# Optimization experiments

Measured on AMD Instinct MI355X. Metric: run time of the kernel, lower is better.

Reference implementation:

```python
import jax, jax.numpy as jnp
import numpy as np
import math

B, S, H = 2, 2048, 2048
NH, LD = 16, 512
HD = H // NH


def setup_inputs() -> dict:
    key = jax.random.key(0)
    ks = jax.random.split(key, 9)
    sc = 0.02
    return {
        "x": jax.random.normal(ks[0], (B, S, H), dtype=jnp.float32),
        "wq": jax.random.normal(ks[1], (H, H), dtype=jnp.float32) * sc,
        "bq": jnp.zeros((H,), dtype=jnp.float32),
        "wk_lat": jax.random.normal(ks[2], (H, LD), dtype=jnp.float32) * sc,
        "wv_lat": jax.random.normal(ks[3], (H, LD), dtype=jnp.float32) * sc,
        "wk": jax.random.normal(ks[4], (LD, H), dtype=jnp.float32) * sc,
        "wv": jax.random.normal(ks[5], (LD, H), dtype=jnp.float32) * sc,
        "wo": jax.random.normal(ks[6], (H, H), dtype=jnp.float32) * sc,
        "bo": jnp.zeros((H,), dtype=jnp.float32),
    }


def reference(x, wq, bq, wk_lat, wv_lat, wk, wv, wo, bo):
    b, s, _ = x.shape
    # projections
    q = (x @ wq + bq).reshape(b, s, NH, HD).transpose(0, 2, 1, 3)  # [B,NH,S,HD]
    k_lat = x @ wk_lat  # [B,S,LD]
    v_lat = x @ wv_lat
    k = (k_lat @ wk).reshape(b, s, NH, HD).transpose(0, 2, 1, 3)
    v = (v_lat @ wv).reshape(b, s, NH, HD).transpose(0, 2, 1, 3)
    # causal attention
    scores = jnp.einsum('bhqd,bhkd->bhqk', q, k) / math.sqrt(HD)
    mask = jnp.tril(jnp.ones((s, s), dtype=bool))  # True = keep
    scores = jnp.where(mask, scores, -jnp.inf)
    weights = jax.nn.softmax(scores, axis=-1)
    out = jnp.einsum('bhqk,bhkd->bhqd', weights, v)
    out = out.transpose(0, 2, 1, 3).reshape(b, s, H)
    return out @ wo + bo
```

## Files before the change

### kernel.cpp

```cpp
#include <hip/hip_runtime.h>
#include <hip/hip_bf16.h>

#define PB   2
#define PS   2048
#define PH   2048
#define PNH  16
#define PLD  512
#define PHD  128
#define PM   (PB * PS)
#define PNCAT 3072
#define ATT_SCALE 0.08838834764831845f
#define ATT_MOFF 4.0f

typedef __attribute__((ext_vector_type(8))) short bf16x8;
typedef __attribute__((ext_vector_type(4))) float f32x4;

__device__ __forceinline__ unsigned short f2bf(float f) {
    unsigned int u = __float_as_uint(f);
    u += 0x7FFFu + ((u >> 16) & 1u);
    return (unsigned short)(u >> 16);
}

__device__ __forceinline__ void gl_lds16(const unsigned short* g, unsigned short* l) {
    __builtin_amdgcn_global_load_lds(
        (const __attribute__((address_space(1))) unsigned int*)g,
        (__attribute__((address_space(3))) unsigned int*)l, 16, 0, 0);
}

#define VMCNT(n)     asm volatile("s_waitcnt vmcnt(" #n ")" ::: "memory")

__global__ __launch_bounds__(256) void cast_f32_bf16_kernel(
    const float* __restrict__ in, unsigned short* __restrict__ out, int n)
{
    int i = (blockIdx.x * 256 + threadIdx.x) * 4;
    if (i >= n) return;
    float4 f = *(const float4*)(in + i);
    unsigned int a = (unsigned int)f2bf(f.x) | ((unsigned int)f2bf(f.y) << 16);
    unsigned int b = (unsigned int)f2bf(f.z) | ((unsigned int)f2bf(f.w) << 16);
    *(uint2*)(out + i) = make_uint2(a, b);
}

__global__ __launch_bounds__(256) void transpose_cast_kernel(
    const float* __restrict__ in, unsigned short* __restrict__ out, int R, int C)
{
    __shared__ float tile[32][33];
    int tx = threadIdx.x, ty = threadIdx.y;
    int r0 = blockIdx.y * 32, c0 = blockIdx.x * 32;
#pragma unroll
    for (int i = 0; i < 32; i += 8)
        tile[ty + i][tx] = in[(size_t)(r0 + ty + i) * C + (c0 + tx)];
    __syncthreads();
#pragma unroll
    for (int i = 0; i < 32; i += 8)
        out[(size_t)(c0 + ty + i) * R + (r0 + tx)] = f2bf(tile[tx][ty + i]);
}

template<int EPI, bool HAS_BIAS>
__global__ __launch_bounds__(256, 3) void gemm97_kernel(
    const unsigned short* __restrict__ A, int lda,
    const unsigned short* __restrict__ BT,
    const float* __restrict__ bias, int nbias,
    void* __restrict__ Cout, int ldc, int K)
{
    __shared__ __align__(16) unsigned short As[128 * 64];
    __shared__ __align__(16) unsigned short Bs[128 * 64];

    const int tid  = threadIdx.x;
    const int wave = tid >> 6, lane = tid & 63;
    const int wm = wave >> 1, wn = wave & 1;
    const int quad = lane >> 4, l15 = lane & 15;
    const int sw = l15 & 7;

    const int gx  = gridDim.x;
    const int nwg = gx * gridDim.y;
    int wg = blockIdx.y * gx + blockIdx.x;
    if (!(nwg & 7)) wg = (wg & 7) * (nwg >> 3) + (wg >> 3);
    const int bm = (wg / gx) * 128, bn = (wg % gx) * 128;

    const int nt = K >> 6;

    const int srow = tid >> 3;
    const int scol = ((tid & 7) ^ (srow & 7)) << 3;
    const unsigned short* Ag = A  + (size_t)(bm + srow) * lda + scol;
    const unsigned short* Bg = BT + (size_t)(bn + srow) * K   + scol;
    unsigned short* const ldsA = &As[wave * 512];
    unsigned short* const ldsB = &Bs[wave * 512];

    auto ldA = [&](int m, int ks) -> bf16x8 {
        int ra = wm * 64 + m * 16 + l15;
        return *(const bf16x8*)&As[ra * 64 + (((ks * 4 + quad) ^ sw) << 3)];
    };
    auto ldB = [&](int j, int ks) -> bf16x8 {
        int rb = wn * 64 + j * 16 + l15;
        return *(const bf16x8*)&Bs[rb * 64 + (((ks * 4 + quad) ^ sw) << 3)];
    };

    f32x4 acc[4][4] = {};

    for (int kt = 0; kt < nt; ++kt) {
        const int k0 = kt * 64;
#pragma unroll
        for (int s = 0; s < 4; ++s) {
            gl_lds16(Ag + (size_t)(s * 32) * lda + k0, ldsA + s * 2048);
            gl_lds16(Bg + (size_t)(s * 32) * K   + k0, ldsB + s * 2048);
        }
        VMCNT(0);
        __syncthreads();

        bf16x8 bfr[4][2];
#pragma unroll
        for (int j = 0; j < 4; ++j)
#pragma unroll
            for (int ks = 0; ks < 2; ++ks) bfr[j][ks] = ldB(j, ks);
#pragma unroll
        for (int m = 0; m < 4; ++m) {
            bf16x8 a0 = ldA(m, 0), a1 = ldA(m, 1);
#pragma unroll
            for (int j = 0; j < 4; ++j) {
                acc[m][j] = __builtin_amdgcn_mfma_f32_16x16x32_bf16(a0, bfr[j][0], acc[m][j], 0, 0, 0);
                acc[m][j] = __builtin_amdgcn_mfma_f32_16x16x32_bf16(a1, bfr[j][1], acc[m][j], 0, 0, 0);
            }
        }
        __syncthreads();
    }

#pragma unroll
    for (int m = 0; m < 4; ++m)
#pragma unroll
        for (int j = 0; j < 4; ++j)
#pragma unroll
            for (int r = 0; r < 4; ++r) {
                int row = bm + wm * 64 + m * 16 + quad * 4 + r;
                int col = bn + wn * 64 + j * 16 + l15;
                float val = acc[m][j][r];
                if (HAS_BIAS && col < nbias) val += bias[col];
                if (EPI == 2) {
                    int bb = row >> 11, s = row & 2047, hh = col >> 7, d = col & 127;
                    size_t idx = ((size_t)((bb << 4) + hh) << 18) + ((size_t)(s >> 6) << 13)
                               + ((d >> 3) << 9) + ((s & 63) << 3) + (d & 7);
                    ((unsigned short*)Cout)[idx] = f2bf(val);
                } else if (EPI == 3) {
                    int bb = row >> 11, s = row & 2047, hh = col >> 7, d = col & 127;
                    size_t idx = ((size_t)((bb << 4) + hh) << 18) + ((size_t)(s >> 6) << 13)
                               + (((s >> 3) & 7) << 10) + (d << 3) + (s & 7);
                    ((unsigned short*)Cout)[idx] = f2bf(val);
                } else if (EPI == 1) {
                    ((float*)Cout)[(size_t)row * ldc + col] = val;
                } else {
                    ((unsigned short*)Cout)[(size_t)row * ldc + col] = f2bf(val);
                }
            }
}

__global__ __launch_bounds__(256) void flash_attn_mfma_kernel(
    const unsigned short* __restrict__ q,
    const unsigned short* __restrict__ kswz,
    const unsigned short* __restrict__ vswz,
    unsigned short* __restrict__ o)
{
    __shared__ __align__(16) unsigned short Kl[2][8192];
    __shared__ __align__(16) unsigned short Vl[8192];
    __shared__ __align__(16) unsigned short Ps[4][16][72];

    const int tid  = threadIdx.x;
    const int wave = tid >> 6;
    const int lane = tid & 63;
    const int quad = lane >> 4, l15 = lane & 15;

    const int bid = blockIdx.x;
    const int qt = 31 - (bid >> 5);
    const int bh = bid & 31;
    const int b  = bh >> 4, h = bh & 15;
    const int q0 = qt * 64;

    const unsigned short* qbase = q + (size_t)(b * PS + q0) * PNCAT + h * PHD;
    const unsigned short* kbase = kswz + ((size_t)bh << 18);
    const unsigned short* vbase = vswz + ((size_t)bh << 18);

    auto stageK = [&](int it, int buf) {
        const unsigned short* kt = kbase + ((size_t)it << 13);
#pragma unroll
        for (int j = 0; j < 4; ++j)
            gl_lds16(kt + (wave * 4 + j) * 512 + lane * 8, &Kl[buf][(wave * 4 + j) * 512]);
    };
    auto stageV = [&](int it) {
        const unsigned short* vt = vbase + ((size_t)it << 13);
#pragma unroll
        for (int j = 0; j < 4; ++j)
            gl_lds16(vt + (wave * 4 + j) * 512 + lane * 8, &Vl[(wave * 4 + j) * 512]);
    };

    bf16x8 aq[4];
#pragma unroll
    for (int kk = 0; kk < 4; ++kk)
        aq[kk] = *(const bf16x8*)(qbase + (size_t)(wave * 16 + l15) * PNCAT + kk * 32 + quad * 8);

    bf16x8 vones;
#pragma unroll
    for (int j = 0; j < 8; ++j) vones[j] = (short)0x3F80;

    f32x4 oacc[8] = {};
    f32x4 lacc = {};

    stageK(0, 0);

    for (int it = 0; it <= qt; ++it) {
        const int cur = it & 1;
        __syncthreads();
        stageV(it);
        if (it < qt) stageK(it + 1, cur ^ 1);

        f32x4 sacc[4] = {};
#pragma unroll
        for (int kk = 0; kk < 4; ++kk)
#pragma unroll
            for (int n = 0; n < 4; ++n) {
                bf16x8 bk = *(const bf16x8*)&Kl[cur][((kk * 4 + quad) * 64 + n * 16 + l15) * 8];
                sacc[n] = __builtin_amdgcn_mfma_f32_16x16x32_bf16(aq[kk], bk, sacc[n], 0, 0, 0);
            }

        const bool diag = (it == qt);
#pragma unroll
        for (int n = 0; n < 4; ++n)
#pragma unroll
            for (int r = 0; r < 4; ++r) {
                float p = __expf(fmaf(sacc[n][r], ATT_SCALE, -ATT_MOFF));
                if (diag && (n * 16 + l15 > wave * 16 + quad * 4 + r)) p = 0.0f;
                Ps[wave][quad * 4 + r][n * 16 + l15] = f2bf(p);
            }

        __syncthreads();

#pragma unroll
        for (int kk = 0; kk < 2; ++kk) {
            bf16x8 ap = *(const bf16x8*)&Ps[wave][l15][kk * 32 + quad * 8];
            lacc = __builtin_amdgcn_mfma_f32_16x16x32_bf16(ap, vones, lacc, 0, 0, 0);
#pragma unroll
            for (int n = 0; n < 8; ++n) {
                bf16x8 bv = *(const bf16x8*)&Vl[((kk * 4 + quad) * 128 + n * 16 + l15) * 8];
                oacc[n] = __builtin_amdgcn_mfma_f32_16x16x32_bf16(ap, bv, oacc[n], 0, 0, 0);
            }
        }
    }

    float inv[4];
#pragma unroll
    for (int r = 0; r < 4; ++r) inv[r] = 1.0f / lacc[r];
#pragma unroll
    for (int n = 0; n < 8; ++n)
#pragma unroll
        for (int r = 0; r < 4; ++r) {
            int row = q0 + wave * 16 + quad * 4 + r;
            int col = h * PHD + n * 16 + l15;
            o[(size_t)(b * PS + row) * PH + col] = f2bf(oacc[n][r] * inv[r]);
        }
}

extern "C" void kernel_launch(void* const* d_in, const int* in_sizes, int n_in,
                              void* d_out, int out_size, void* d_ws, size_t ws_size,
                              hipStream_t stream)
{
    const float* x      = (const float*)d_in[0];
    const float* wq     = (const float*)d_in[1];
    const float* bq     = (const float*)d_in[2];
    const float* wk_lat = (const float*)d_in[3];
    const float* wv_lat = (const float*)d_in[4];
    const float* wk     = (const float*)d_in[5];
    const float* wv     = (const float*)d_in[6];
    const float* wo     = (const float*)d_in[7];
    const float* bo     = (const float*)d_in[8];
    float* out = (float*)d_out;

    char* ws = (char*)d_ws;
    size_t off = 0;
    auto alloc = [&](size_t bytes) -> void* {
        void* p = ws + off;
        off += (bytes + 255) & ~(size_t)255;
        return p;
    };
    unsigned short* xb    = (unsigned short*)alloc((size_t)PM * PH * 2);
    unsigned short* wcatT = (unsigned short*)alloc((size_t)PNCAT * PH * 2);
    unsigned short* wkT   = (unsigned short*)alloc((size_t)PH * PLD * 2);
    unsigned short* wvT   = (unsigned short*)alloc((size_t)PH * PLD * 2);
    unsigned short* woT   = (unsigned short*)alloc((size_t)PH * PH * 2);
    unsigned short* cat   = (unsigned short*)alloc((size_t)PM * PNCAT * 2);
    unsigned short* kswz  = (unsigned short*)alloc((size_t)PM * PH * 2);
    unsigned short* attn  = (unsigned short*)alloc((size_t)PM * PH * 2);
    unsigned short* vswz  = xb;

    unsigned short* wqT    = wcatT;
    unsigned short* wkLatT = wcatT + (size_t)PH * PH;
    unsigned short* wvLatT = wcatT + (size_t)(PH + PLD) * PH;

    dim3 tb(32, 8);

    cast_f32_bf16_kernel<<<(PM * PH) / 4 / 256, 256, 0, stream>>>(x, xb, PM * PH);
    transpose_cast_kernel<<<dim3(PH / 32,  PH / 32),  tb, 0, stream>>>(wq,     wqT,    PH,  PH);
    transpose_cast_kernel<<<dim3(PLD / 32, PH / 32),  tb, 0, stream>>>(wk_lat, wkLatT, PH,  PLD);
    transpose_cast_kernel<<<dim3(PLD / 32, PH / 32),  tb, 0, stream>>>(wv_lat, wvLatT, PH,  PLD);
    transpose_cast_kernel<<<dim3(PH / 32,  PLD / 32), tb, 0, stream>>>(wk,     wkT,    PLD, PH);
    transpose_cast_kernel<<<dim3(PH / 32,  PLD / 32), tb, 0, stream>>>(wv,     wvT,    PLD, PH);
    transpose_cast_kernel<<<dim3(PH / 32,  PH / 32),  tb, 0, stream>>>(wo,     woT,    PH,  PH);

    gemm97_kernel<0, true><<<dim3(PNCAT / 128, PM / 128), 256, 0, stream>>>(
        xb, PH, wcatT, bq, PH, cat, PNCAT, PH);

    gemm97_kernel<2, false><<<dim3(PH / 128, PM / 128), 256, 0, stream>>>(
        cat + PH, PNCAT, wkT, nullptr, 0, kswz, 0, PLD);
    gemm97_kernel<3, false><<<dim3(PH / 128, PM / 128), 256, 0, stream>>>(
        cat + PH + PLD, PNCAT, wvT, nullptr, 0, vswz, 0, PLD);

    flash_attn_mfma_kernel<<<PB * PNH * (PS / 64), 256, 0, stream>>>(cat, kswz, vswz, attn);

    gemm97_kernel<1, true><<<dim3(PH / 128, PM / 128), 256, 0, stream>>>(
        attn, PH, woT, bo, PH, out, PH, PH);
}
```

Baseline: 343.5 us.

## Single-buffer K in attention for occupancy, use exp2, batch weight transposes into one launch

The attention kernel drops double-buffered K staging and loads K and V together at the start of each tile. This shrinks LDS so three blocks can fit per CU, as the new launch bounds request, but it gives up the K prefetch overlap. The exponent now uses exp2f with pre-scaled constants, and the Ps row padding goes from 72 to 76. The six weight transpose-cast launches are merged into one 3D-grid kernel that reads its parameters from a struct, cutting launch overhead at the cost of early-exiting blocks for the smaller matrices.

```diff
diff --git a/kernel.cpp b/kernel.cpp
--- a/kernel.cpp
+++ b/kernel.cpp
@@ -11,6 +11,8 @@
 #define PNCAT 3072
 #define ATT_SCALE 0.08838834764831845f
 #define ATT_MOFF 4.0f
+#define ATT_SC2  0.12751744f
+#define ATT_MO2  5.77078016f
 
 typedef __attribute__((ext_vector_type(8))) short bf16x8;
 typedef __attribute__((ext_vector_type(4))) float f32x4;
@@ -28,6 +30,7 @@
 }
 
 #define VMCNT(n)     asm volatile("s_waitcnt vmcnt(" #n ")" ::: "memory")
+#define MEMFENCE()   asm volatile("" ::: "memory")
 
 __global__ __launch_bounds__(256) void cast_f32_bf16_kernel(
     const float* __restrict__ in, unsigned short* __restrict__ out, int n)
@@ -40,12 +43,23 @@
     *(uint2*)(out + i) = make_uint2(a, b);
 }
 
-__global__ __launch_bounds__(256) void transpose_cast_kernel(
-    const float* __restrict__ in, unsigned short* __restrict__ out, int R, int C)
+struct TC6 {
+    const float* src[6];
+    unsigned short* dst[6];
+    int R[6];
+    int C[6];
+};
+
+__global__ __launch_bounds__(256) void transpose_cast6_kernel(TC6 p)
 {
     __shared__ float tile[32][33];
+    const int z = blockIdx.z;
+    const int r0 = blockIdx.y * 32, c0 = blockIdx.x * 32;
+    const int R = p.R[z], C = p.C[z];
+    if (r0 >= R || c0 >= C) return;
+    const float* in = p.src[z];
+    unsigned short* out = p.dst[z];
     int tx = threadIdx.x, ty = threadIdx.y;
-    int r0 = blockIdx.y * 32, c0 = blockIdx.x * 32;
 #pragma unroll
     for (int i = 0; i < 32; i += 8)
         tile[ty + i][tx] = in[(size_t)(r0 + ty + i) * C + (c0 + tx)];
@@ -152,15 +166,15 @@
             }
 }
 
-__global__ __launch_bounds__(256) void flash_attn_mfma_kernel(
+__global__ __launch_bounds__(256, 3) void flash_attn_mfma_kernel(
     const unsigned short* __restrict__ q,
     const unsigned short* __restrict__ kswz,
     const unsigned short* __restrict__ vswz,
     unsigned short* __restrict__ o)
 {
-    __shared__ __align__(16) unsigned short Kl[2][8192];
+    __shared__ __align__(16) unsigned short Kl[8192];
     __shared__ __align__(16) unsigned short Vl[8192];
-    __shared__ __align__(16) unsigned short Ps[4][16][72];
+    __shared__ __align__(16) unsigned short Ps[4][16][76];
 
     const int tid  = threadIdx.x;
     const int wave = tid >> 6;
@@ -177,11 +191,11 @@
     const unsigned short* kbase = kswz + ((size_t)bh << 18);
     const unsigned short* vbase = vswz + ((size_t)bh << 18);
 
-    auto stageK = [&](int it, int buf) {
+    auto stageK = [&](int it) {
         const unsigned short* kt = kbase + ((size_t)it << 13);
 #pragma unroll
         for (int j = 0; j < 4; ++j)
-            gl_lds16(kt + (wave * 4 + j) * 512 + lane * 8, &Kl[buf][(wave * 4 + j) * 512]);
+            gl_lds16(kt + (wave * 4 + j) * 512 + lane * 8, &Kl[(wave * 4 + j) * 512]);
     };
     auto stageV = [&](int it) {
         const unsigned short* vt = vbase + ((size_t)it << 13);
@@ -202,20 +216,20 @@
     f32x4 oacc[8] = {};
     f32x4 lacc = {};
 
-    stageK(0, 0);
-
     for (int it = 0; it <= qt; ++it) {
-        const int cur = it & 1;
         __syncthreads();
+        stageK(it);
         stageV(it);
-        if (it < qt) stageK(it + 1, cur ^ 1);
+        VMCNT(4);
+        __builtin_amdgcn_s_barrier();
+        MEMFENCE();
 
         f32x4 sacc[4] = {};
 #pragma unroll
         for (int kk = 0; kk < 4; ++kk)
 #pragma unroll
             for (int n = 0; n < 4; ++n) {
-                bf16x8 bk = *(const bf16x8*)&Kl[cur][((kk * 4 + quad) * 64 + n * 16 + l15) * 8];
+                bf16x8 bk = *(const bf16x8*)&Kl[((kk * 4 + quad) * 64 + n * 16 + l15) * 8];
                 sacc[n] = __builtin_amdgcn_mfma_f32_16x16x32_bf16(aq[kk], bk, sacc[n], 0, 0, 0);
             }
 
@@ -224,7 +238,7 @@
         for (int n = 0; n < 4; ++n)
 #pragma unroll
             for (int r = 0; r < 4; ++r) {
-                float p = __expf(fmaf(sacc[n][r], ATT_SCALE, -ATT_MOFF));
+                float p = exp2f(fmaf(sacc[n][r], ATT_SC2, -ATT_MO2));
                 if (diag && (n * 16 + l15 > wave * 16 + quad * 4 + r)) p = 0.0f;
                 Ps[wave][quad * 4 + r][n * 16 + l15] = f2bf(p);
             }
@@ -292,15 +306,16 @@
     unsigned short* wkLatT = wcatT + (size_t)PH * PH;
     unsigned short* wvLatT = wcatT + (size_t)(PH + PLD) * PH;
 
-    dim3 tb(32, 8);
-
     cast_f32_bf16_kernel<<<(PM * PH) / 4 / 256, 256, 0, stream>>>(x, xb, PM * PH);
-    transpose_cast_kernel<<<dim3(PH / 32,  PH / 32),  tb, 0, stream>>>(wq,     wqT,    PH,  PH);
-    transpose_cast_kernel<<<dim3(PLD / 32, PH / 32),  tb, 0, stream>>>(wk_lat, wkLatT, PH,  PLD);
-    transpose_cast_kernel<<<dim3(PLD / 32, PH / 32),  tb, 0, stream>>>(wv_lat, wvLatT, PH,  PLD);
-    transpose_cast_kernel<<<dim3(PH / 32,  PLD / 32), tb, 0, stream>>>(wk,     wkT,    PLD, PH);
-    transpose_cast_kernel<<<dim3(PH / 32,  PLD / 32), tb, 0, stream>>>(wv,     wvT,    PLD, PH);
-    transpose_cast_kernel<<<dim3(PH / 32,  PH / 32),  tb, 0, stream>>>(wo,     woT,    PH,  PH);
+
+    TC6 tc;
+    tc.src[0] = wq;     tc.dst[0] = wqT;    tc.R[0] = PH;  tc.C[0] = PH;
+    tc.src[1] = wk_lat; tc.dst[1] = wkLatT; tc.R[1] = PH;  tc.C[1] = PLD;
+    tc.src[2] = wv_lat; tc.dst[2] = wvLatT; tc.R[2] = PH;  tc.C[2] = PLD;
+    tc.src[3] = wk;     tc.dst[3] = wkT;    tc.R[3] = PLD; tc.C[3] = PH;
+    tc.src[4] = wv;     tc.dst[4] = wvT;    tc.R[4] = PLD; tc.C[4] = PH;
+    tc.src[5] = wo;     tc.dst[5] = woT;    tc.R[5] = PH;  tc.C[5] = PH;
+    transpose_cast6_kernel<<<dim3(64, 64, 6), dim3(32, 8), 0, stream>>>(tc);
 
     gemm97_kernel<0, true><<<dim3(PNCAT / 128, PM / 128), 256, 0, stream>>>(
         xb, PH, wcatT, bq, PH, cat, PNCAT, PH);
```

Result: no change. 337.1 us (-1.9%).
